# Kernel optimization log

Hardware: AMD Instinct MI355X
Metric: run time of the kernel (lower is better)

The kernel has to match this reference:

```python
import jax, jax.numpy as jnp
import numpy as np
import math

B, L, D, H = 4, 2048, 1024, 16
HD = D // H
EPS = 1e-5


def setup_inputs() -> dict:
    key = jax.random.key(0)
    ks = jax.random.split(key, 6)
    s = 1.0 / math.sqrt(D)
    return {
        "x": jax.random.normal(ks[0], (B, L, D), dtype=jnp.float32),
        "Wq": jax.random.normal(ks[1], (D, D), dtype=jnp.float32) * s,
        "bq": jnp.zeros((D,), jnp.float32),
        "Wk": jax.random.normal(ks[2], (D, D), dtype=jnp.float32) * s,
        "bk": jnp.zeros((D,), jnp.float32),
        "Wv": jax.random.normal(ks[3], (D, D), dtype=jnp.float32) * s,
        "bv": jnp.zeros((D,), jnp.float32),
        "Wo": jax.random.normal(ks[4], (D, D), dtype=jnp.float32) * s,
        "bo": jnp.zeros((D,), jnp.float32),
        "gamma": jnp.ones((D,), jnp.float32),
        "beta": jnp.zeros((D,), jnp.float32),
    }


def reference(x, Wq, bq, Wk, bk, Wv, bv, Wo, bo, gamma, beta):
    # projections -> [B, H, L, HD]
    def split_heads(t):
        return t.reshape(B, L, H, HD).transpose(0, 2, 1, 3)

    q = split_heads(x @ Wq + bq)
    k = split_heads(x @ Wk + bk)
    v = split_heads(x @ Wv + bv)

    scores = jnp.einsum("bhqd,bhkd->bhqk", q, k) / math.sqrt(HD)
    attn = jax.nn.softmax(scores, axis=-1)  # dropout p=0.0 -> identity
    out = jnp.einsum("bhqk,bhkd->bhqd", attn, v)
    out = out.transpose(0, 2, 1, 3).reshape(B, L, D)
    out = out @ Wo + bo

    # residual + LayerNorm
    y = x + out
    mu = jnp.mean(y, axis=-1, keepdims=True)
    var = jnp.mean(jnp.square(y - mu), axis=-1, keepdims=True)
    return (y - mu) * jax.lax.rsqrt(var + EPS) * gamma + beta
```

## Files before the change

kernel.cpp:

```cpp
#include <hip/hip_runtime.h>

typedef unsigned short u16;
typedef short v8s __attribute__((ext_vector_type(8)));
typedef float v4f __attribute__((ext_vector_type(4)));

#define BB 4
#define LL 2048
#define DD 1024
#define NH 16
#define HD 64
#define QSCALE 0.18033688011112042f
#define PAD 72

__device__ __forceinline__ float bf2f(u16 u) {
  union { unsigned int i; float f; } v; v.i = ((unsigned int)u) << 16; return v.f;
}
__device__ __forceinline__ u16 f2bf(float f) {
  union { float f; unsigned int i; } v; v.f = f;
  unsigned int u = v.i;
  return (u16)((u + 0x7fffu + ((u >> 16) & 1u)) >> 16);
}
__device__ __forceinline__ void gl_lds16(const u16* g, u16* l) {
  __builtin_amdgcn_global_load_lds(
      (const __attribute__((address_space(1))) void*)g,
      (__attribute__((address_space(3))) void*)l, 16, 0, 0);
}

__global__ __launch_bounds__(256) void fill_val(float* __restrict__ out, float v, int n) {
  int i = blockIdx.x * 256 + threadIdx.x;
  if (i < n) out[i] = v;
}

__global__ __launch_bounds__(256) void cast_x(
    const float* __restrict__ x, u16* __restrict__ Xb) {
  int i = (blockIdx.x * 256 + threadIdx.x) * 8;
  float4 a = *(const float4*)(x + i);
  float4 b = *(const float4*)(x + i + 4);
  v8s v;
  v[0] = (short)f2bf(a.x); v[1] = (short)f2bf(a.y);
  v[2] = (short)f2bf(a.z); v[3] = (short)f2bf(a.w);
  v[4] = (short)f2bf(b.x); v[5] = (short)f2bf(b.y);
  v[6] = (short)f2bf(b.z); v[7] = (short)f2bf(b.w);
  *(v8s*)(Xb + i) = v;
}

__global__ __launch_bounds__(256) void transpose_w(
    const float* __restrict__ Wq, const float* __restrict__ Wk,
    const float* __restrict__ Wv, const float* __restrict__ Wo,
    u16* __restrict__ WT) {
  __shared__ u16 tile[64][72];
  int z = blockIdx.z;
  const float* src = (z == 0) ? Wq : (z == 1) ? Wk : (z == 2) ? Wv : Wo;
  u16* dst = WT + (size_t)z * DD * DD;
  int n0 = blockIdx.x * 64, k0 = blockIdx.y * 64;
  int tid = threadIdx.x;
#pragma unroll
  for (int i = 0; i < 2; ++i) {
    int cid = i * 256 + tid;
    int r = cid >> 3, c = (cid & 7) * 8;
    const float* sp = src + (size_t)(k0 + r) * DD + n0 + c;
    float4 a = *(const float4*)sp;
    float4 b = *(const float4*)(sp + 4);
    tile[r][c + 0] = f2bf(a.x); tile[r][c + 1] = f2bf(a.y);
    tile[r][c + 2] = f2bf(a.z); tile[r][c + 3] = f2bf(a.w);
    tile[r][c + 4] = f2bf(b.x); tile[r][c + 5] = f2bf(b.y);
    tile[r][c + 6] = f2bf(b.z); tile[r][c + 7] = f2bf(b.w);
  }
  __syncthreads();
#pragma unroll
  for (int i = 0; i < 2; ++i) {
    int cid = i * 256 + tid;
    int r = cid >> 3, c = (cid & 7) * 8;
    v8s v;
#pragma unroll
    for (int j = 0; j < 8; ++j) v[j] = (short)tile[c + j][r];
    *(v8s*)(dst + (size_t)(n0 + r) * DD + k0 + c) = v;
  }
}

__global__ __launch_bounds__(256) void gemm128(
    const u16* __restrict__ Xb, const u16* __restrict__ CTX,
    const u16* __restrict__ WT,
    const float* __restrict__ bq, const float* __restrict__ bk,
    const float* __restrict__ bv, const float* __restrict__ bo,
    u16* __restrict__ Qb, u16* __restrict__ Kb, u16* __restrict__ Vtb,
    u16* __restrict__ projb, int nbase) {
  __shared__ __align__(16) u16 As[128 * 64];
  __shared__ __align__(16) u16 Bs[128 * 64];

  int tid = threadIdx.x;
  int wave = tid >> 6, lane = tid & 63, quad = lane >> 4, l15 = lane & 15;
  int wr = wave >> 1, wc = wave & 1;
  int bx = blockIdx.x + nbase;
  int mode = bx >> 3;
  int n0g = bx * 128;
  int m0 = blockIdx.y * 128;
  const float* bias = (mode == 0) ? bq : (mode == 1) ? bk : (mode == 2) ? bv : bo;

  const u16* Ab = ((mode == 3) ? CTX : Xb) + (size_t)m0 * DD;
  const u16* Bb = WT + (size_t)n0g * DD;
  int lrow = lane >> 3, lcol = (lane & 7) * 8;

  v4f acc[4][4] = {};

  for (int kt = 0; kt < DD / 64; ++kt) {
    int k0 = kt * 64;
    __syncthreads();
#pragma unroll
    for (int j = 0; j < 4; ++j) {
      int seg = wave * 4 + j;
      gl_lds16(Ab + (size_t)(seg * 8 + lrow) * DD + k0 + lcol, &As[seg * 512]);
      gl_lds16(Bb + (size_t)(seg * 8 + lrow) * DD + k0 + lcol, &Bs[seg * 512]);
    }
    __syncthreads();

#pragma unroll
    for (int cc = 0; cc < 2; ++cc) {
      v8s a[4], b[4];
#pragma unroll
      for (int i = 0; i < 4; ++i)
        a[i] = *(const v8s*)&As[(wr * 64 + i * 16 + l15) * 64 + cc * 32 + quad * 8];
#pragma unroll
      for (int j = 0; j < 4; ++j)
        b[j] = *(const v8s*)&Bs[(wc * 64 + j * 16 + l15) * 64 + cc * 32 + quad * 8];
#pragma unroll
      for (int i = 0; i < 4; ++i)
#pragma unroll
        for (int j = 0; j < 4; ++j)
          acc[i][j] = __builtin_amdgcn_mfma_f32_16x16x32_bf16(a[i], b[j], acc[i][j], 0, 0, 0);
    }
  }

#pragma unroll
  for (int j = 0; j < 4; ++j) {
    int n_g = n0g + wc * 64 + j * 16 + l15;
    int n = n_g & (DD - 1);
    float bias_v = bias[n];
#pragma unroll
    for (int i = 0; i < 4; ++i)
#pragma unroll
      for (int r = 0; r < 4; ++r) {
        int m = m0 + wr * 64 + i * 16 + quad * 4 + r;
        float v = acc[i][j][r] + bias_v;
        if (mode == 3) {
          projb[(size_t)m * DD + n] = f2bf(v);
        } else {
          int b = m >> 11, l = m & (LL - 1);
          int h = n >> 6, d = n & 63;
          if (mode == 0) {
            Qb[((size_t)(b * NH + h) * LL + l) * HD + d] = f2bf(v * QSCALE);
          } else if (mode == 1) {
            Kb[((size_t)(b * NH + h) * LL + l) * HD + d] = f2bf(v);
          } else {
            Vtb[((size_t)(b * NH + h) * HD + d) * LL + l] = f2bf(v);
          }
        }
      }
  }
}

__global__ __launch_bounds__(256) void attn(
    const u16* __restrict__ Qb, const u16* __restrict__ Kb,
    const u16* __restrict__ Vtb, u16* __restrict__ ctx) {
  __shared__ __align__(16) u16 Ks[64 * PAD];
  __shared__ __align__(16) u16 Vs[64 * PAD];
  __shared__ __align__(16) u16 Ps[4][16 * PAD];

  int tid = threadIdx.x;
  int wave = tid >> 6, lane = tid & 63, quad = lane >> 4, l15 = lane & 15;
  int bh = blockIdx.y;
  int q0 = blockIdx.x * 128;

  v8s aq[2][2];
#pragma unroll
  for (int s2 = 0; s2 < 2; ++s2) {
    const u16* Qp = Qb + ((size_t)bh * LL + q0 + s2 * 64 + wave * 16 + l15) * HD;
    aq[s2][0] = *(const v8s*)(Qp + quad * 8);
    aq[s2][1] = *(const v8s*)(Qp + 32 + quad * 8);
  }

  v4f o[2][4] = {};
  float ls[2][4] = {};

  const u16* Kbase = Kb + (size_t)bh * LL * HD;
  const u16* Vbase = Vtb + (size_t)bh * HD * LL;

  for (int kt = 0; kt < LL / 64; ++kt) {
    int k0 = kt * 64;
    __syncthreads();
#pragma unroll
    for (int i = 0; i < 2; ++i) {
      int cid = i * 256 + tid;
      int r = cid >> 3, c = (cid & 7) * 8;
      *(v8s*)&Ks[r * PAD + c] = *(const v8s*)(Kbase + (size_t)(k0 + r) * HD + c);
      *(v8s*)&Vs[r * PAD + c] = *(const v8s*)(Vbase + (size_t)r * LL + k0 + c);
    }
    __syncthreads();

    v4f s[2][4];
#pragma unroll
    for (int t = 0; t < 4; ++t) {
      v8s b0 = *(const v8s*)&Ks[(t * 16 + l15) * PAD + quad * 8];
      v8s b1 = *(const v8s*)&Ks[(t * 16 + l15) * PAD + 32 + quad * 8];
#pragma unroll
      for (int s2 = 0; s2 < 2; ++s2) {
        v4f z = {};
        z = __builtin_amdgcn_mfma_f32_16x16x32_bf16(aq[s2][0], b0, z, 0, 0, 0);
        s[s2][t] = __builtin_amdgcn_mfma_f32_16x16x32_bf16(aq[s2][1], b1, z, 0, 0, 0);
      }
    }

#pragma unroll
    for (int s2 = 0; s2 < 2; ++s2) {
#pragma unroll
      for (int t = 0; t < 4; ++t)
#pragma unroll
        for (int r = 0; r < 4; ++r) {
          float p = exp2f(s[s2][t][r] - 64.f);
          ls[s2][r] += p;
          union { float f; unsigned int i; } u; u.f = p;
          Ps[wave][(quad * 4 + r) * PAD + t * 16 + l15] =
              (u16)((u.i + 0x8000u) >> 16);
        }
      v8s ap0 = *(const v8s*)&Ps[wave][l15 * PAD + quad * 8];
      v8s ap1 = *(const v8s*)&Ps[wave][l15 * PAD + 32 + quad * 8];
#pragma unroll
      for (int t = 0; t < 4; ++t) {
        v8s vb0 = *(const v8s*)&Vs[(t * 16 + l15) * PAD + quad * 8];
        v8s vb1 = *(const v8s*)&Vs[(t * 16 + l15) * PAD + 32 + quad * 8];
        o[s2][t] = __builtin_amdgcn_mfma_f32_16x16x32_bf16(ap0, vb0, o[s2][t], 0, 0, 0);
        o[s2][t] = __builtin_amdgcn_mfma_f32_16x16x32_bf16(ap1, vb1, o[s2][t], 0, 0, 0);
      }
    }
  }

  int b = bh >> 4, h = bh & 15;
#pragma unroll
  for (int s2 = 0; s2 < 2; ++s2)
#pragma unroll
    for (int r = 0; r < 4; ++r) {
      float v = ls[s2][r];
      v += __shfl_xor(v, 1); v += __shfl_xor(v, 2);
      v += __shfl_xor(v, 4); v += __shfl_xor(v, 8);
      float inv = 1.f / v;
      int l = q0 + s2 * 64 + wave * 16 + quad * 4 + r;
#pragma unroll
      for (int t = 0; t < 4; ++t)
        ctx[((size_t)(b * LL + l)) * DD + h * HD + t * 16 + l15] =
            f2bf(o[s2][t][r] * inv);
    }
}

__global__ __launch_bounds__(256) void resid_ln(
    const float* __restrict__ x, const u16* __restrict__ projb,
    const float* __restrict__ gamma, const float* __restrict__ beta,
    float* __restrict__ out) {
  int row = blockIdx.x, tid = threadIdx.x;
  int base = tid * 4;
  float4 xv = *(const float4*)(x + (size_t)row * DD + base);
  ushort4 pv = *(const ushort4*)(projb + (size_t)row * DD + base);
  float y0 = xv.x + bf2f(pv.x), y1 = xv.y + bf2f(pv.y);
  float y2 = xv.z + bf2f(pv.z), y3 = xv.w + bf2f(pv.w);

  float s = y0 + y1 + y2 + y3;
  s += __shfl_xor(s, 1);  s += __shfl_xor(s, 2);  s += __shfl_xor(s, 4);
  s += __shfl_xor(s, 8);  s += __shfl_xor(s, 16); s += __shfl_xor(s, 32);
  __shared__ float red[8];
  int wv = tid >> 6, ln = tid & 63;
  if (ln == 0) red[wv] = s;
  __syncthreads();
  float mu = (red[0] + red[1] + red[2] + red[3]) * (1.f / DD);

  float d0 = y0 - mu, d1 = y1 - mu, d2 = y2 - mu, d3 = y3 - mu;
  float vv = d0 * d0 + d1 * d1 + d2 * d2 + d3 * d3;
  vv += __shfl_xor(vv, 1);  vv += __shfl_xor(vv, 2);  vv += __shfl_xor(vv, 4);
  vv += __shfl_xor(vv, 8);  vv += __shfl_xor(vv, 16); vv += __shfl_xor(vv, 32);
  if (ln == 0) red[4 + wv] = vv;
  __syncthreads();
  float var = (red[4] + red[5] + red[6] + red[7]) * (1.f / DD);
  float rstd = rsqrtf(var + 1e-5f);

  float4 gv = *(const float4*)(gamma + base);
  float4 bv = *(const float4*)(beta + base);
  float4 ov;
  ov.x = d0 * rstd * gv.x + bv.x;
  ov.y = d1 * rstd * gv.y + bv.y;
  ov.z = d2 * rstd * gv.z + bv.z;
  ov.w = d3 * rstd * gv.w + bv.w;
  *(float4*)(out + (size_t)row * DD + base) = ov;
}

extern "C" void kernel_launch(void* const* d_in, const int* in_sizes, int n_in,
                              void* d_out, int out_size, void* d_ws, size_t ws_size,
                              hipStream_t stream) {
  (void)ws_size;
  float* out = (float*)d_out;

  bool ok = (n_in == 11) && (out_size == BB * LL * DD);
  if (ok) {
    const int want[11] = {BB * LL * DD, DD * DD, DD, DD * DD, DD, DD * DD,
                          DD, DD * DD, DD, DD, DD};
    for (int i = 0; i < 11; ++i) ok = ok && (in_sizes[i] == want[i]);
  }
  if (!ok) {
    fill_val<<<(out_size + 255) / 256, 256, 0, stream>>>(out, 1000.0f, out_size);
    return;
  }

  const float* x     = (const float*)d_in[0];
  const float* Wq    = (const float*)d_in[1];
  const float* bq    = (const float*)d_in[2];
  const float* Wk    = (const float*)d_in[3];
  const float* bk    = (const float*)d_in[4];
  const float* Wv    = (const float*)d_in[5];
  const float* bv    = (const float*)d_in[6];
  const float* Wo    = (const float*)d_in[7];
  const float* bo    = (const float*)d_in[8];
  const float* gamma = (const float*)d_in[9];
  const float* beta  = (const float*)d_in[10];

  char* ws = (char*)d_ws;
  u16* WT   = (u16*)(ws);
  u16* Xb   = (u16*)(ws + (size_t)8 * 1024 * 1024);
  u16* Qb   = (u16*)(ws + (size_t)24 * 1024 * 1024);
  u16* Kb   = (u16*)(ws + (size_t)40 * 1024 * 1024);
  u16* Vtb  = (u16*)(ws + (size_t)56 * 1024 * 1024);
  u16* ctxO = (u16*)d_out;
  u16* projb = Xb;

  cast_x<<<4096, 256, 0, stream>>>(x, Xb);
  transpose_w<<<dim3(16, 16, 4), 256, 0, stream>>>(Wq, Wk, Wv, Wo, WT);
  gemm128<<<dim3(24, 64), 256, 0, stream>>>(Xb, ctxO, WT, bq, bk, bv, bo,
                                            Qb, Kb, Vtb, projb, 0);
  attn<<<dim3(LL / 128, BB * NH), 256, 0, stream>>>(Qb, Kb, Vtb, ctxO);
  gemm128<<<dim3(8, 64), 256, 0, stream>>>(Xb, ctxO, WT, bq, bk, bv, bo,
                                           Qb, Kb, Vtb, projb, 24);
  resid_ln<<<8192, 256, 0, stream>>>(x, projb, gamma, beta, out);
}
```

Measured before the change: 384.9 us.

## Keep attention probabilities in registers via transposed QK^T and permlane swaps

Computes S^T (K as A operand, Q as B operand) so each lane holds probabilities along the key dimension. It then packs them to bf16 with v_cvt_pk_bf16_f32 and uses permlane32/16 swaps to build the P·V A-operand directly in registers. This removes the per-wave LDS round trip for P and the scattered 2-byte LDS stores. It also changes the row-sum reduction to a per-lane sum with cross-quad shuffles, and adds an occupancy hint to launch_bounds. The risks are more register pressure and reliance on gfx950-specific permlane instructions whose lane-mapping correctness is subtle.

```diff
diff --git a/kernel.cpp b/kernel.cpp
--- a/kernel.cpp
+++ b/kernel.cpp
@@ -3,6 +3,7 @@
 typedef unsigned short u16;
 typedef short v8s __attribute__((ext_vector_type(8)));
 typedef float v4f __attribute__((ext_vector_type(4)));
+typedef unsigned int v4u __attribute__((ext_vector_type(4)));
 
 #define BB 4
 #define LL 2048
@@ -24,6 +25,17 @@
   __builtin_amdgcn_global_load_lds(
       (const __attribute__((address_space(1))) void*)g,
       (__attribute__((address_space(3))) void*)l, 16, 0, 0);
+}
+__device__ __forceinline__ unsigned cvtpk_bf16(float lo, float hi) {
+  unsigned r;
+  asm("v_cvt_pk_bf16_f32 %0, %1, %2" : "=v"(r) : "v"(lo), "v"(hi));
+  return r;
+}
+__device__ __forceinline__ void pl32swap(unsigned& a, unsigned& b) {
+  asm("v_permlane32_swap_b32 %0, %1" : "+v"(a), "+v"(b));
+}
+__device__ __forceinline__ void pl16swap(unsigned& a, unsigned& b) {
+  asm("v_permlane16_swap_b32 %0, %1" : "+v"(a), "+v"(b));
 }
 
 __global__ __launch_bounds__(256) void fill_val(float* __restrict__ out, float v, int n) {
@@ -159,12 +171,11 @@
   }
 }
 
-__global__ __launch_bounds__(256) void attn(
+__global__ __launch_bounds__(256, 4) void attn(
     const u16* __restrict__ Qb, const u16* __restrict__ Kb,
     const u16* __restrict__ Vtb, u16* __restrict__ ctx) {
   __shared__ __align__(16) u16 Ks[64 * PAD];
   __shared__ __align__(16) u16 Vs[64 * PAD];
-  __shared__ __align__(16) u16 Ps[4][16 * PAD];
 
   int tid = threadIdx.x;
   int wave = tid >> 6, lane = tid & 63, quad = lane >> 4, l15 = lane & 15;
@@ -180,7 +191,7 @@
   }
 
   v4f o[2][4] = {};
-  float ls[2][4] = {};
+  float ls2[2] = {0.f, 0.f};
 
   const u16* Kbase = Kb + (size_t)bh * LL * HD;
   const u16* Vbase = Vtb + (size_t)bh * HD * LL;
@@ -197,58 +208,78 @@
     }
     __syncthreads();
 
-    v4f s[2][4];
+    v8s ak[4][2];
 #pragma unroll
     for (int t = 0; t < 4; ++t) {
-      v8s b0 = *(const v8s*)&Ks[(t * 16 + l15) * PAD + quad * 8];
-      v8s b1 = *(const v8s*)&Ks[(t * 16 + l15) * PAD + 32 + quad * 8];
+      ak[t][0] = *(const v8s*)&Ks[(t * 16 + l15) * PAD + quad * 8];
+      ak[t][1] = *(const v8s*)&Ks[(t * 16 + l15) * PAD + 32 + quad * 8];
+    }
+
+    v8s ap[2][2];
+#pragma unroll
+    for (int s2 = 0; s2 < 2; ++s2) {
+      v4f s[4];
+#pragma unroll
+      for (int t = 0; t < 4; ++t) {
+        v4f z = {};
+        z = __builtin_amdgcn_mfma_f32_16x16x32_bf16(ak[t][0], aq[s2][0], z, 0, 0, 0);
+        s[t] = __builtin_amdgcn_mfma_f32_16x16x32_bf16(ak[t][1], aq[s2][1], s[t] = z, 0, 0, 0);
+      }
+      unsigned W[4][2];
+      float psum = 0.f;
+#pragma unroll
+      for (int t = 0; t < 4; ++t) {
+        float p0 = __builtin_amdgcn_exp2f(s[t][0] - 64.f);
+        float p1 = __builtin_amdgcn_exp2f(s[t][1] - 64.f);
+        float p2 = __builtin_amdgcn_exp2f(s[t][2] - 64.f);
+        float p3 = __builtin_amdgcn_exp2f(s[t][3] - 64.f);
+        psum += (p0 + p1) + (p2 + p3);
+        W[t][0] = cvtpk_bf16(p0, p1);
+        W[t][1] = cvtpk_bf16(p2, p3);
+      }
+      ls2[s2] += psum;
+      union { v4u u; v8s s8; } c0, c1;
+#pragma unroll
+      for (int j = 0; j < 2; ++j) {
+        unsigned a = W[0][j], b = W[1][j];
+        pl32swap(a, b); pl16swap(a, b);
+        c0.u[j] = a; c0.u[2 + j] = b;
+        unsigned a2 = W[2][j], b2 = W[3][j];
+        pl32swap(a2, b2); pl16swap(a2, b2);
+        c1.u[j] = a2; c1.u[2 + j] = b2;
+      }
+      ap[s2][0] = c0.s8; ap[s2][1] = c1.s8;
+    }
+
+#pragma unroll
+    for (int t = 0; t < 4; ++t) {
+      v8s vb0 = *(const v8s*)&Vs[(t * 16 + l15) * PAD + quad * 8];
+      v8s vb1 = *(const v8s*)&Vs[(t * 16 + l15) * PAD + 32 + quad * 8];
 #pragma unroll
       for (int s2 = 0; s2 < 2; ++s2) {
-        v4f z = {};
-        z = __builtin_amdgcn_mfma_f32_16x16x32_bf16(aq[s2][0], b0, z, 0, 0, 0);
-        s[s2][t] = __builtin_amdgcn_mfma_f32_16x16x32_bf16(aq[s2][1], b1, z, 0, 0, 0);
-      }
-    }
-
-#pragma unroll
-    for (int s2 = 0; s2 < 2; ++s2) {
-#pragma unroll
-      for (int t = 0; t < 4; ++t)
-#pragma unroll
-        for (int r = 0; r < 4; ++r) {
-          float p = exp2f(s[s2][t][r] - 64.f);
-          ls[s2][r] += p;
-          union { float f; unsigned int i; } u; u.f = p;
-          Ps[wave][(quad * 4 + r) * PAD + t * 16 + l15] =
-              (u16)((u.i + 0x8000u) >> 16);
-        }
-      v8s ap0 = *(const v8s*)&Ps[wave][l15 * PAD + quad * 8];
-      v8s ap1 = *(const v8s*)&Ps[wave][l15 * PAD + 32 + quad * 8];
-#pragma unroll
-      for (int t = 0; t < 4; ++t) {
-        v8s vb0 = *(const v8s*)&Vs[(t * 16 + l15) * PAD + quad * 8];
-        v8s vb1 = *(const v8s*)&Vs[(t * 16 + l15) * PAD + 32 + quad * 8];
-        o[s2][t] = __builtin_amdgcn_mfma_f32_16x16x32_bf16(ap0, vb0, o[s2][t], 0, 0, 0);
-        o[s2][t] = __builtin_amdgcn_mfma_f32_16x16x32_bf16(ap1, vb1, o[s2][t], 0, 0, 0);
+        o[s2][t] = __builtin_amdgcn_mfma_f32_16x16x32_bf16(ap[s2][0], vb0, o[s2][t], 0, 0, 0);
+        o[s2][t] = __builtin_amdgcn_mfma_f32_16x16x32_bf16(ap[s2][1], vb1, o[s2][t], 0, 0, 0);
       }
     }
   }
 
   int b = bh >> 4, h = bh & 15;
 #pragma unroll
-  for (int s2 = 0; s2 < 2; ++s2)
+  for (int s2 = 0; s2 < 2; ++s2) {
+    float tot = ls2[s2];
+    tot += __shfl_xor(tot, 16);
+    tot += __shfl_xor(tot, 32);
+    float recip = 1.f / tot;
 #pragma unroll
     for (int r = 0; r < 4; ++r) {
-      float v = ls[s2][r];
-      v += __shfl_xor(v, 1); v += __shfl_xor(v, 2);
-      v += __shfl_xor(v, 4); v += __shfl_xor(v, 8);
-      float inv = 1.f / v;
+      float inv = __shfl(recip, quad * 4 + r);
       int l = q0 + s2 * 64 + wave * 16 + quad * 4 + r;
 #pragma unroll
       for (int t = 0; t < 4; ++t)
         ctx[((size_t)(b * LL + l)) * DD + h * HD + t * 16 + l15] =
             f2bf(o[s2][t][r] * inv);
     }
+  }
 }
 
 __global__ __launch_bounds__(256) void resid_ln(
```

After: 344.3 us. -10.5%, faster.
